# Optimization experiments

Hardware: AMD Instinct MI355X
Metric: run time of the kernel (lower is better)

Reference implementation:

```python
import jax, jax.numpy as jnp
import numpy as np

D = 8  # polynomial degree; with bias present, basis has D columns (P1..PD)


def setup_inputs() -> dict:
    key = jax.random.key(0)
    k1, k2 = jax.random.split(key)
    batch, n_in, n_out = 65536, 256, 64
    x = jax.random.normal(k1, (batch, n_in), dtype=jnp.float32)
    c_basis = jax.random.normal(k2, (n_out, n_in, D), dtype=jnp.float32) * (1.0 / np.sqrt(n_in * D))
    bias = jnp.zeros((n_out,), dtype=jnp.float32)
    return {"x": x, "c_basis": c_basis, "bias": bias}


def _legendre_basis(x):
    # x: (batch, n_in). Returns (batch, n_in, D) = [P1(t), ..., PD(t)], t = tanh(x).
    t = jnp.tanh(x)
    p_prev = jnp.ones_like(t)  # P0
    p_curr = t                 # P1
    polys = [p_curr]
    for k in range(2, D + 1):  # small fixed-length loop over degree
        p_next = ((2 * k - 1) * t * p_curr - (k - 1) * p_prev) / k
        polys.append(p_next)
        p_prev, p_curr = p_curr, p_next
    return jnp.stack(polys, axis=-1)  # (batch, n_in, D)


def reference(x, c_basis, bias):
    # basis: (batch, n_in, D); contract over (n_in, D) with c_basis (n_out, n_in, D)
    leg = _legendre_basis(x)
    y = jnp.einsum('bid,oid->bo', leg, c_basis)
    return y + bias
```

## Files before the change

### kernel.cpp

```cpp
#include <hip/hip_runtime.h>
#include <hip/hip_bf16.h>

typedef __attribute__((ext_vector_type(8))) short short8;
typedef __attribute__((ext_vector_type(4))) float floatx4;
typedef __attribute__((ext_vector_type(4))) unsigned int uintx4;

#define GLOBAL_AS __attribute__((address_space(1)))
#define LDS_AS __attribute__((address_space(3)))

__device__ __forceinline__ void async_ld16(const void* g, void* l) {
  __builtin_amdgcn_global_load_lds((const GLOBAL_AS unsigned int*)g,
                                   (LDS_AS unsigned int*)l, 16, 0, 0);
}

__device__ __forceinline__ unsigned pack2_bf16_rn(float a, float b) {
  __hip_bfloat162 h = __float22bfloat162_rn(make_float2(a, b));
  unsigned r;
  __builtin_memcpy(&r, &h, 4);
  return r;
}

__device__ __forceinline__ unsigned pack2_bf16_fast(float a, float b) {
  unsigned ua, ub;
  __builtin_memcpy(&ua, &a, 4);
  __builtin_memcpy(&ub, &b, 4);
  return __builtin_amdgcn_perm(ub + 0x8000u, ua + 0x8000u, 0x07060302u);
}

__device__ __forceinline__ short8 legendre_frag(float xv) {
  float e  = __builtin_amdgcn_exp2f(xv * 2.885390081777927f);
  float t  = 1.0f - 2.0f * __builtin_amdgcn_rcpf(e + 1.0f);
  float p1 = t;
  float u2 = t * p1,  w2 = u2 - 1.0f;  float p2 = fmaf(0.5f, w2, u2);
  float u3 = t * p2,  w3 = u3 - p1;    float p3 = fmaf(2.0f/3.0f, w3, u3);
  float u4 = t * p3,  w4 = u4 - p2;    float p4 = fmaf(0.75f, w4, u4);
  float u5 = t * p4,  w5 = u5 - p3;    float p5 = fmaf(0.8f, w5, u5);
  float u6 = t * p5,  w6 = u6 - p4;    float p6 = fmaf(5.0f/6.0f, w6, u6);
  float u7 = t * p6,  w7 = u7 - p5;    float p7 = fmaf(6.0f/7.0f, w7, u7);
  float u8 = t * p7,  w8 = u8 - p6;    float p8 = fmaf(7.0f/8.0f, w8, u8);
  union { unsigned u[4]; short8 s; } r;
  r.u[0] = pack2_bf16_fast(p1, p2);
  r.u[1] = pack2_bf16_fast(p3, p4);
  r.u[2] = pack2_bf16_fast(p5, p6);
  r.u[3] = pack2_bf16_fast(p7, p8);
  return r.s;
}

__global__ void conv_kernel(const float* __restrict__ cb, unsigned short* __restrict__ ws) {
  int t = blockIdx.x * 256 + threadIdx.x;
  int o = t >> 8;
  int i = t & 255;
  const floatx4* s = (const floatx4*)(cb + ((size_t)o * 256 + i) * 8);
  floatx4 v0 = s[0], v1 = s[1];
  uintx4 w;
  w.x = pack2_bf16_rn(v0.x, v0.y);
  w.y = pack2_bf16_rn(v0.z, v0.w);
  w.z = pack2_bf16_rn(v1.x, v1.y);
  w.w = pack2_bf16_rn(v1.z, v1.w);
  *(uintx4*)(ws + (size_t)i * 512 + o * 8) = w;
}

#define MB 128
#define NCH 16

__global__ __launch_bounds__(256, 2) void kan_kernel(
    const float* __restrict__ x, const unsigned short* __restrict__ ws,
    const float* __restrict__ bias, float* __restrict__ y) {
  __shared__ __align__(16) unsigned short bt[2][16 * 64 * 8];
  __shared__ __align__(16) float xs[2][MB * 16];

  const int tid  = threadIdx.x;
  const int wid  = tid >> 6;
  const int lane = tid & 63;
  const int m    = lane & 15;
  const int q    = lane >> 4;
  const int row_block = blockIdx.x * MB;

  floatx4 acc[2][4];
#pragma unroll
  for (int a = 0; a < 2; ++a)
#pragma unroll
    for (int nt = 0; nt < 4; ++nt) acc[a][nt] = (floatx4){0.f, 0.f, 0.f, 0.f};

  auto stage = [&](int ch, int buf) {
#pragma unroll
    for (int t = 0; t < 4; ++t) {
      int sb = t * 256 + wid * 64;
      async_ld16(ws + (size_t)ch * 8192 + (size_t)(sb + lane) * 8, &bt[buf][sb * 8]);
    }
#pragma unroll
    for (int t = 0; t < 2; ++t) {
      int sb = t * 256 + wid * 64;
      int slot = sb + lane;
      int r = slot >> 2;
      int c4 = (slot & 3) ^ (r & 3);
      async_ld16(x + (size_t)(row_block + r) * 256 + ch * 16 + c4 * 4, &xs[buf][sb * 4]);
    }
  };

  const int xoff0 = (wid * 32 + m) * 64 + ((m & 3) << 4) + q * 4;
  const int xoff1 = xoff0 + 16 * 64;

  stage(0, 0);
#pragma unroll 2
  for (int ch = 0; ch < NCH; ++ch) {
    const int buf = ch & 1;
    asm volatile("s_barrier" ::: "memory");
    if (ch + 1 < NCH) {
      stage(ch + 1, buf ^ 1);
      asm volatile("s_waitcnt vmcnt(6)" ::: "memory");
    } else {
      asm volatile("s_waitcnt vmcnt(0)" ::: "memory");
    }

    const unsigned short* bp = &bt[buf][q * 512 + m * 8];
    const char* xb = (const char*)&xs[buf][0];
#pragma unroll
    for (int ks = 0; ks < 4; ++ks) {
      short8 fb0 = *(const short8*)(bp + ks * 2048 + 0 * 128);
      short8 fb1 = *(const short8*)(bp + ks * 2048 + 1 * 128);
      short8 fb2 = *(const short8*)(bp + ks * 2048 + 2 * 128);
      short8 fb3 = *(const short8*)(bp + ks * 2048 + 3 * 128);
      float xv0 = *(const float*)(xb + (xoff0 ^ (ks << 4)));
      float xv1 = *(const float*)(xb + (xoff1 ^ (ks << 4)));
      short8 fa0 = legendre_frag(xv0);
      short8 fa1 = legendre_frag(xv1);
      acc[0][0] = __builtin_amdgcn_mfma_f32_16x16x32_bf16(fa0, fb0, acc[0][0], 0, 0, 0);
      acc[1][0] = __builtin_amdgcn_mfma_f32_16x16x32_bf16(fa1, fb0, acc[1][0], 0, 0, 0);
      acc[0][1] = __builtin_amdgcn_mfma_f32_16x16x32_bf16(fa0, fb1, acc[0][1], 0, 0, 0);
      acc[1][1] = __builtin_amdgcn_mfma_f32_16x16x32_bf16(fa1, fb1, acc[1][1], 0, 0, 0);
      acc[0][2] = __builtin_amdgcn_mfma_f32_16x16x32_bf16(fa0, fb2, acc[0][2], 0, 0, 0);
      acc[1][2] = __builtin_amdgcn_mfma_f32_16x16x32_bf16(fa1, fb2, acc[1][2], 0, 0, 0);
      acc[0][3] = __builtin_amdgcn_mfma_f32_16x16x32_bf16(fa0, fb3, acc[0][3], 0, 0, 0);
      acc[1][3] = __builtin_amdgcn_mfma_f32_16x16x32_bf16(fa1, fb3, acc[1][3], 0, 0, 0);
    }
  }

  float bv[4];
#pragma unroll
  for (int nt = 0; nt < 4; ++nt) bv[nt] = bias[nt * 16 + m];
#pragma unroll
  for (int a = 0; a < 2; ++a) {
    int gr0 = row_block + wid * 32 + a * 16 + q * 4;
#pragma unroll
    for (int nt = 0; nt < 4; ++nt) {
#pragma unroll
      for (int r = 0; r < 4; ++r) {
        y[(size_t)(gr0 + r) * 64 + nt * 16 + m] = acc[a][nt][r] + bv[nt];
      }
    }
  }
}

extern "C" void kernel_launch(void* const* d_in, const int* in_sizes, int n_in,
                              void* d_out, int out_size, void* d_ws, size_t ws_size,
                              hipStream_t stream) {
  const float* x    = (const float*)d_in[0];
  const float* cb   = (const float*)d_in[1];
  const float* bias = (const float*)d_in[2];
  float* y = (float*)d_out;
  unsigned short* ws = (unsigned short*)d_ws;
  int batch = in_sizes[0] / 256;
  hipLaunchKernelGGL(conv_kernel, dim3(64), dim3(256), 0, stream, cb, ws);
  hipLaunchKernelGGL(kan_kernel, dim3(batch / MB), dim3(256), 0, stream, x, ws, bias, y);
}
```

Before: 123.3 us.

## Switch Legendre basis to packed fp16 math and halve block size

Computes the Legendre recurrence in packed half2 arithmetic, evaluating two rows per instruction, and feeds fp16 MFMA instead of bf16. Weights are converted to fp16. Blocks shrink to 128 threads and 64 rows, with precomputed staging pointers and an extra barrier after the async wait. The aim is to cut the VALU cost of basis generation. In exchange, fp16 recurrence accumulation may lose accuracy, and smaller blocks restage the full weight tile per 64 rows, which doubles LDS traffic for weights.

```diff
diff --git a/kernel.cpp b/kernel.cpp
--- a/kernel.cpp
+++ b/kernel.cpp
@@ -1,7 +1,8 @@
 #include <hip/hip_runtime.h>
 #include <hip/hip_bf16.h>
 
-typedef __attribute__((ext_vector_type(8))) short short8;
+typedef _Float16 half2v __attribute__((ext_vector_type(2)));
+typedef _Float16 half8  __attribute__((ext_vector_type(8)));
 typedef __attribute__((ext_vector_type(4))) float floatx4;
 typedef __attribute__((ext_vector_type(4))) unsigned int uintx4;
 
@@ -13,60 +14,62 @@
                                    (LDS_AS unsigned int*)l, 16, 0, 0);
 }
 
-__device__ __forceinline__ unsigned pack2_bf16_rn(float a, float b) {
-  __hip_bfloat162 h = __float22bfloat162_rn(make_float2(a, b));
-  unsigned r;
-  __builtin_memcpy(&r, &h, 4);
-  return r;
+__device__ __forceinline__ half2v h2(float v) {
+  return (half2v){(_Float16)v, (_Float16)v};
 }
 
-__device__ __forceinline__ unsigned pack2_bf16_fast(float a, float b) {
-  unsigned ua, ub;
-  __builtin_memcpy(&ua, &a, 4);
-  __builtin_memcpy(&ub, &b, 4);
-  return __builtin_amdgcn_perm(ub + 0x8000u, ua + 0x8000u, 0x07060302u);
+__device__ __forceinline__ void legendre2_f16(float xv0, float xv1,
+                                              half8* fa0, half8* fa1) {
+  float e0 = __builtin_amdgcn_exp2f(xv0 * 2.885390081777927f);
+  float t0 = 1.0f - 2.0f * __builtin_amdgcn_rcpf(e0 + 1.0f);
+  float e1 = __builtin_amdgcn_exp2f(xv1 * 2.885390081777927f);
+  float t1 = 1.0f - 2.0f * __builtin_amdgcn_rcpf(e1 + 1.0f);
+  half2v t;
+  { auto tt = __builtin_amdgcn_cvt_pkrtz(t0, t1); __builtin_memcpy(&t, &tt, 4); }
+  half2v p1 = t;
+  half2v u2 = t * p1, w2 = u2 - h2(1.0f);  half2v p2 = h2(0.5f)      * w2 + u2;
+  half2v u3 = t * p2, w3 = u3 - p1;        half2v p3 = h2(2.0f/3.0f) * w3 + u3;
+  half2v u4 = t * p3, w4 = u4 - p2;        half2v p4 = h2(0.75f)     * w4 + u4;
+  half2v u5 = t * p4, w5 = u5 - p3;        half2v p5 = h2(0.8f)      * w5 + u5;
+  half2v u6 = t * p5, w6 = u6 - p4;        half2v p6 = h2(5.0f/6.0f) * w6 + u6;
+  half2v u7 = t * p6, w7 = u7 - p5;        half2v p7 = h2(6.0f/7.0f) * w7 + u7;
+  half2v u8 = t * p7, w8 = u8 - p6;        half2v p8 = h2(7.0f/8.0f) * w8 + u8;
+  unsigned P[8];
+  __builtin_memcpy(&P[0], &p1, 4); __builtin_memcpy(&P[1], &p2, 4);
+  __builtin_memcpy(&P[2], &p3, 4); __builtin_memcpy(&P[3], &p4, 4);
+  __builtin_memcpy(&P[4], &p5, 4); __builtin_memcpy(&P[5], &p6, 4);
+  __builtin_memcpy(&P[6], &p7, 4); __builtin_memcpy(&P[7], &p8, 4);
+  union { unsigned u[4]; half8 h; } a0, a1;
+#pragma unroll
+  for (int j = 0; j < 4; ++j) {
+    a0.u[j] = __builtin_amdgcn_perm(P[2*j+1], P[2*j], 0x05040100u);
+    a1.u[j] = __builtin_amdgcn_perm(P[2*j+1], P[2*j], 0x07060302u);
+  }
+  *fa0 = a0.h;
+  *fa1 = a1.h;
 }
 
-__device__ __forceinline__ short8 legendre_frag(float xv) {
-  float e  = __builtin_amdgcn_exp2f(xv * 2.885390081777927f);
-  float t  = 1.0f - 2.0f * __builtin_amdgcn_rcpf(e + 1.0f);
-  float p1 = t;
-  float u2 = t * p1,  w2 = u2 - 1.0f;  float p2 = fmaf(0.5f, w2, u2);
-  float u3 = t * p2,  w3 = u3 - p1;    float p3 = fmaf(2.0f/3.0f, w3, u3);
-  float u4 = t * p3,  w4 = u4 - p2;    float p4 = fmaf(0.75f, w4, u4);
-  float u5 = t * p4,  w5 = u5 - p3;    float p5 = fmaf(0.8f, w5, u5);
-  float u6 = t * p5,  w6 = u6 - p4;    float p6 = fmaf(5.0f/6.0f, w6, u6);
-  float u7 = t * p6,  w7 = u7 - p5;    float p7 = fmaf(6.0f/7.0f, w7, u7);
-  float u8 = t * p7,  w8 = u8 - p6;    float p8 = fmaf(7.0f/8.0f, w8, u8);
-  union { unsigned u[4]; short8 s; } r;
-  r.u[0] = pack2_bf16_fast(p1, p2);
-  r.u[1] = pack2_bf16_fast(p3, p4);
-  r.u[2] = pack2_bf16_fast(p5, p6);
-  r.u[3] = pack2_bf16_fast(p7, p8);
-  return r.s;
-}
-
-__global__ void conv_kernel(const float* __restrict__ cb, unsigned short* __restrict__ ws) {
-  int t = blockIdx.x * 256 + threadIdx.x;
+__global__ void conv_kernel(const float* __restrict__ cb, _Float16* __restrict__ ws) {
+  int t = blockIdx.x * 128 + threadIdx.x;
   int o = t >> 8;
   int i = t & 255;
   const floatx4* s = (const floatx4*)(cb + ((size_t)o * 256 + i) * 8);
   floatx4 v0 = s[0], v1 = s[1];
-  uintx4 w;
-  w.x = pack2_bf16_rn(v0.x, v0.y);
-  w.y = pack2_bf16_rn(v0.z, v0.w);
-  w.z = pack2_bf16_rn(v1.x, v1.y);
-  w.w = pack2_bf16_rn(v1.z, v1.w);
-  *(uintx4*)(ws + (size_t)i * 512 + o * 8) = w;
+  union { _Float16 h[8]; uintx4 u; } w;
+  w.h[0] = (_Float16)v0.x; w.h[1] = (_Float16)v0.y;
+  w.h[2] = (_Float16)v0.z; w.h[3] = (_Float16)v0.w;
+  w.h[4] = (_Float16)v1.x; w.h[5] = (_Float16)v1.y;
+  w.h[6] = (_Float16)v1.z; w.h[7] = (_Float16)v1.w;
+  *(uintx4*)(ws + (size_t)i * 512 + o * 8) = w.u;
 }
 
-#define MB 128
+#define MB 64
 #define NCH 16
 
-__global__ __launch_bounds__(256, 2) void kan_kernel(
-    const float* __restrict__ x, const unsigned short* __restrict__ ws,
+__global__ __launch_bounds__(128, 2) void kan_kernel(
+    const float* __restrict__ x, const _Float16* __restrict__ ws,
     const float* __restrict__ bias, float* __restrict__ y) {
-  __shared__ __align__(16) unsigned short bt[2][16 * 64 * 8];
+  __shared__ __align__(16) _Float16 bt[2][16 * 64 * 8];
   __shared__ __align__(16) float xs[2][MB * 16];
 
   const int tid  = threadIdx.x;
@@ -82,57 +85,70 @@
 #pragma unroll
     for (int nt = 0; nt < 4; ++nt) acc[a][nt] = (floatx4){0.f, 0.f, 0.f, 0.f};
 
-  auto stage = [&](int ch, int buf) {
+  const _Float16* bsrc[8];
 #pragma unroll
-    for (int t = 0; t < 4; ++t) {
-      int sb = t * 256 + wid * 64;
-      async_ld16(ws + (size_t)ch * 8192 + (size_t)(sb + lane) * 8, &bt[buf][sb * 8]);
+  for (int t = 0; t < 8; ++t)
+    bsrc[t] = ws + (size_t)(t * 128 + wid * 64 + lane) * 8;
+  const float* xsrc[2];
+#pragma unroll
+  for (int t = 0; t < 2; ++t) {
+    int slot = t * 128 + wid * 64 + lane;
+    int r = slot >> 2;
+    int c4 = (slot & 3) ^ (r & 3);
+    xsrc[t] = x + (size_t)(row_block + r) * 256 + c4 * 4;
+  }
+
+  auto stage = [&](int buf) {
+#pragma unroll
+    for (int t = 0; t < 8; ++t) {
+      int sb = t * 128 + wid * 64;
+      async_ld16(bsrc[t], &bt[buf][sb * 8]);
+      bsrc[t] += 8192;
     }
 #pragma unroll
     for (int t = 0; t < 2; ++t) {
-      int sb = t * 256 + wid * 64;
-      int slot = sb + lane;
-      int r = slot >> 2;
-      int c4 = (slot & 3) ^ (r & 3);
-      async_ld16(x + (size_t)(row_block + r) * 256 + ch * 16 + c4 * 4, &xs[buf][sb * 4]);
+      int sb = t * 128 + wid * 64;
+      async_ld16(xsrc[t], &xs[buf][sb * 4]);
+      xsrc[t] += 16;
     }
   };
 
   const int xoff0 = (wid * 32 + m) * 64 + ((m & 3) << 4) + q * 4;
-  const int xoff1 = xoff0 + 16 * 64;
+  const int xoff1 = xoff0 + 1024;
 
-  stage(0, 0);
+  stage(0);
 #pragma unroll 2
   for (int ch = 0; ch < NCH; ++ch) {
     const int buf = ch & 1;
     asm volatile("s_barrier" ::: "memory");
     if (ch + 1 < NCH) {
-      stage(ch + 1, buf ^ 1);
-      asm volatile("s_waitcnt vmcnt(6)" ::: "memory");
+      stage(buf ^ 1);
+      asm volatile("s_waitcnt vmcnt(10)" ::: "memory");
     } else {
       asm volatile("s_waitcnt vmcnt(0)" ::: "memory");
     }
+    asm volatile("s_barrier" ::: "memory");
 
-    const unsigned short* bp = &bt[buf][q * 512 + m * 8];
+    const _Float16* bp = &bt[buf][q * 512 + m * 8];
     const char* xb = (const char*)&xs[buf][0];
 #pragma unroll
     for (int ks = 0; ks < 4; ++ks) {
-      short8 fb0 = *(const short8*)(bp + ks * 2048 + 0 * 128);
-      short8 fb1 = *(const short8*)(bp + ks * 2048 + 1 * 128);
-      short8 fb2 = *(const short8*)(bp + ks * 2048 + 2 * 128);
-      short8 fb3 = *(const short8*)(bp + ks * 2048 + 3 * 128);
+      half8 fb0 = *(const half8*)(bp + ks * 2048 + 0 * 128);
+      half8 fb1 = *(const half8*)(bp + ks * 2048 + 1 * 128);
+      half8 fb2 = *(const half8*)(bp + ks * 2048 + 2 * 128);
+      half8 fb3 = *(const half8*)(bp + ks * 2048 + 3 * 128);
       float xv0 = *(const float*)(xb + (xoff0 ^ (ks << 4)));
       float xv1 = *(const float*)(xb + (xoff1 ^ (ks << 4)));
-      short8 fa0 = legendre_frag(xv0);
-      short8 fa1 = legendre_frag(xv1);
-      acc[0][0] = __builtin_amdgcn_mfma_f32_16x16x32_bf16(fa0, fb0, acc[0][0], 0, 0, 0);
-      acc[1][0] = __builtin_amdgcn_mfma_f32_16x16x32_bf16(fa1, fb0, acc[1][0], 0, 0, 0);
-      acc[0][1] = __builtin_amdgcn_mfma_f32_16x16x32_bf16(fa0, fb1, acc[0][1], 0, 0, 0);
-      acc[1][1] = __builtin_amdgcn_mfma_f32_16x16x32_bf16(fa1, fb1, acc[1][1], 0, 0, 0);
-      acc[0][2] = __builtin_amdgcn_mfma_f32_16x16x32_bf16(fa0, fb2, acc[0][2], 0, 0, 0);
-      acc[1][2] = __builtin_amdgcn_mfma_f32_16x16x32_bf16(fa1, fb2, acc[1][2], 0, 0, 0);
-      acc[0][3] = __builtin_amdgcn_mfma_f32_16x16x32_bf16(fa0, fb3, acc[0][3], 0, 0, 0);
-      acc[1][3] = __builtin_amdgcn_mfma_f32_16x16x32_bf16(fa1, fb3, acc[1][3], 0, 0, 0);
+      half8 fa0, fa1;
+      legendre2_f16(xv0, xv1, &fa0, &fa1);
+      acc[0][0] = __builtin_amdgcn_mfma_f32_16x16x32_f16(fa0, fb0, acc[0][0], 0, 0, 0);
+      acc[1][0] = __builtin_amdgcn_mfma_f32_16x16x32_f16(fa1, fb0, acc[1][0], 0, 0, 0);
+      acc[0][1] = __builtin_amdgcn_mfma_f32_16x16x32_f16(fa0, fb1, acc[0][1], 0, 0, 0);
+      acc[1][1] = __builtin_amdgcn_mfma_f32_16x16x32_f16(fa1, fb1, acc[1][1], 0, 0, 0);
+      acc[0][2] = __builtin_amdgcn_mfma_f32_16x16x32_f16(fa0, fb2, acc[0][2], 0, 0, 0);
+      acc[1][2] = __builtin_amdgcn_mfma_f32_16x16x32_f16(fa1, fb2, acc[1][2], 0, 0, 0);
+      acc[0][3] = __builtin_amdgcn_mfma_f32_16x16x32_f16(fa0, fb3, acc[0][3], 0, 0, 0);
+      acc[1][3] = __builtin_amdgcn_mfma_f32_16x16x32_f16(fa1, fb3, acc[1][3], 0, 0, 0);
     }
   }
 
@@ -159,8 +175,8 @@
   const float* cb   = (const float*)d_in[1];
   const float* bias = (const float*)d_in[2];
   float* y = (float*)d_out;
-  unsigned short* ws = (unsigned short*)d_ws;
+  _Float16* ws = (_Float16*)d_ws;
   int batch = in_sizes[0] / 256;
-  hipLaunchKernelGGL(conv_kernel, dim3(64), dim3(256), 0, stream, cb, ws);
-  hipLaunchKernelGGL(kan_kernel, dim3(batch / MB), dim3(256), 0, stream, x, ws, bias, y);
+  hipLaunchKernelGGL(conv_kernel, dim3(128), dim3(128), 0, stream, cb, ws);
+  hipLaunchKernelGGL(kan_kernel, dim3(batch / MB), dim3(128), 0, stream, x, ws, bias, y);
 }
```

Result: faster. 120.4 us (-2.3%).
